# Optimization experiments

Hardware: AMD Instinct MI355X
Metric: run time of the kernel (lower is better)

Reference implementation:

```python
import jax, jax.numpy as jnp
import numpy as np
import math

D_MODEL = 512
N_HEADS = 8
D_K = D_MODEL // N_HEADS
N_SAMPLES = 16
BETA = 1.0
SCALE = 1.0 / math.sqrt(D_K)
PROPOSAL_TEMP = 0.5


def setup_inputs() -> dict:
    key = jax.random.key(0)
    ks = jax.random.split(key, 9)
    B, S = 2, 512
    x = jax.random.normal(ks[0], (B, S, D_MODEL), dtype=jnp.float32)
    init = lambda k: jax.random.normal(k, (D_MODEL, D_MODEL), dtype=jnp.float32) * 0.02
    return {
        "x": x,
        "Wq": init(ks[1]), "bq": jnp.zeros((D_MODEL,), jnp.float32),
        "Wk": init(ks[2]), "bk": jnp.zeros((D_MODEL,), jnp.float32),
        "Wv": init(ks[3]), "bv": jnp.zeros((D_MODEL,), jnp.float32),
        "Wo": init(ks[4]), "bo": jnp.zeros((D_MODEL,), jnp.float32),
    }


def _importance_sampled_weights(scores):
    # scores: [B,H,S,S]. Replicates the per-row Python loop, fully vectorized.
    B, H, Sq, Sk = scores.shape
    target = jax.nn.softmax(scores * BETA, axis=-1)            # [B,H,Sq,Sk]
    # optimal proposal: 0.5*target + 0.5*uniform
    prop = PROPOSAL_TEMP * target + (1.0 - PROPOSAL_TEMP) / Sk
    R = B * H * Sq
    tf = target.reshape(R, Sk)
    pf = prop.reshape(R, Sk)
    # tsu_backend.sample_binary_layer(log(p/(1-p))) == Bernoulli(p) sampling
    s = jax.random.bernoulli(jax.random.key(42), pf[:, None, :], (R, N_SAMPLES, Sk))
    # importance weight = prod(target[sel]) / (prod(prop[sel]) * prod(1-prop[~sel]))
    pt = jnp.prod(jnp.where(s, tf[:, None, :], 1.0), axis=-1)                 # [R,N]
    pp = jnp.prod(jnp.where(s, pf[:, None, :], 1.0 - pf[:, None, :]), axis=-1)
    valid = (s.sum(-1) > 0) & (pp > 0)
    w = jnp.where(valid, pt / jnp.maximum(pp, 1e-38), 0.0)
    ws = w.sum(-1, keepdims=True)
    w = jnp.where(ws > 0, w / jnp.maximum(ws, 1e-38), 1.0 / N_SAMPLES)        # [R,N]
    wa = jnp.einsum('rn,rnk->rk', w, s.astype(jnp.float32))                   # [R,Sk]
    was = wa.sum(-1, keepdims=True)
    wa = jnp.where(was > 0, wa / jnp.maximum(was, 1e-38), 1.0 / Sk)
    return wa.reshape(B, H, Sq, Sk)


def reference(x, Wq, bq, Wk, bk, Wv, bv, Wo, bo):
    B, S, Dm = x.shape
    proj = lambda W, b: (x @ W + b).reshape(B, S, N_HEADS, D_K).transpose(0, 2, 1, 3)
    Q = proj(Wq, bq)  # [B,H,S,dk]
    K = proj(Wk, bk)
    V = proj(Wv, bv)
    scores = jnp.einsum('bhqd,bhkd->bhqk', Q, K) * SCALE
    # torch builds weights via torch.tensor(...) which detaches => constant w.r.t. params
    attn = jax.lax.stop_gradient(_importance_sampled_weights(scores))
    out = jnp.einsum('bhqk,bhkd->bhqd', attn, V)
    out = out.transpose(0, 2, 1, 3).reshape(B, S, Dm)
    return out @ Wo + bo
```

## Files before the change

### kernel.cpp

```cpp
#include <hip/hip_runtime.h>
#include <cstdint>
#include <cstddef>


#if __has_builtin(__builtin_amdgcn_alignbit)
#define ROTL(x, r) __builtin_amdgcn_alignbit((x), (x), 32 - (r))
#else
#define ROTL(x, r) (((x) << (r)) | ((x) >> (32 - (r))))
#endif

__device__ __forceinline__ void tf4_fold(uint32_t ca, uint32_t cb, uint32_t cc,
                                         uint32_t cd, uint32_t &ra,
                                         uint32_t &rb, uint32_t &rc,
                                         uint32_t &rd) {
  uint32_t a0 = 0u, a1 = ca, b0 = 0u, b1 = cb;
  uint32_t c0 = 0u, c1 = cc, d0 = 0u, d1 = cd;
#define QR(s)                                                                 \
  a0 += a1; b0 += b1; c0 += c1; d0 += d1;                                     \
  a1 = ROTL(a1, s); b1 = ROTL(b1, s); c1 = ROTL(c1, s); d1 = ROTL(d1, s);     \
  a1 ^= a0; b1 ^= b0; c1 ^= c0; d1 ^= d0;
#define INJ(x, y)                                                             \
  a0 += (x); b0 += (x); c0 += (x); d0 += (x);                                 \
  a1 += (y); b1 += (y); c1 += (y); d1 += (y);
  QR(13) QR(15) QR(26) QR(6)
  INJ(42u, 0x1BD11BF1u)
  QR(17) QR(29) QR(16) QR(24)
  INJ(0x1BD11BF0u, 2u)
  QR(13) QR(15) QR(26) QR(6)
  a1 += 45u; b1 += 45u; c1 += 45u; d1 += 45u;
  QR(17) QR(29) QR(16) QR(24)
  INJ(42u, 0x1BD11BF4u)
  QR(13) QR(15) QR(26) QR(6)
  INJ(0x1BD11BF0u, 5u)
#undef QR
#undef INJ
  ra = a0 ^ a1; rb = b0 ^ b1; rc = c0 ^ c1; rd = d0 ^ d1;
}

__global__ __launch_bounds__(256)
void qkv_gemm(const float* __restrict__ x,
              const float* __restrict__ Wq, const float* __restrict__ bq,
              const float* __restrict__ Wk, const float* __restrict__ bk,
              const float* __restrict__ Wv, const float* __restrict__ bv,
              float* __restrict__ Qw, float* __restrict__ Kw,
              float* __restrict__ Vw) {
  const float* W; const float* bias; float* out;
  if (blockIdx.z == 0)      { W = Wq; bias = bq; out = Qw; }
  else if (blockIdx.z == 1) { W = Wk; bias = bk; out = Kw; }
  else                      { W = Wv; bias = bv; out = Vw; }

  __shared__ float At[32][68];
  __shared__ float Bs[32][64];
  const int tid = threadIdx.x;
  const int tx = tid & 15, ty = tid >> 4;
  const int row0 = blockIdx.x * 64, col0 = blockIdx.y * 64;
  float acc[4][4] = {};

  for (int kk = 0; kk < 512; kk += 32) {
    const int ar = tid >> 2;
#pragma unroll
    for (int i = 0; i < 2; ++i) {
      const int kc = ((tid & 3) << 3) + (i << 2);
      const float4 a4 =
          *(const float4*)&x[(size_t)(row0 + ar) * 512 + kk + kc];
      At[kc + 0][ar] = a4.x; At[kc + 1][ar] = a4.y;
      At[kc + 2][ar] = a4.z; At[kc + 3][ar] = a4.w;
    }
#pragma unroll
    for (int i = 0; i < 2; ++i) {
      const int idx = tid + (i << 8);
      const int br = idx >> 4, bc = (idx & 15) << 2;
      *(float4*)&Bs[br][bc] =
          *(const float4*)&W[(size_t)(kk + br) * 512 + col0 + bc];
    }
    __syncthreads();
#pragma unroll
    for (int p = 0; p < 32; ++p) {
      const float4 a4 = *(const float4*)&At[p][ty << 2];
      const float4 b4 = *(const float4*)&Bs[p][tx << 2];
      acc[0][0] = fmaf(a4.x, b4.x, acc[0][0]); acc[0][1] = fmaf(a4.x, b4.y, acc[0][1]);
      acc[0][2] = fmaf(a4.x, b4.z, acc[0][2]); acc[0][3] = fmaf(a4.x, b4.w, acc[0][3]);
      acc[1][0] = fmaf(a4.y, b4.x, acc[1][0]); acc[1][1] = fmaf(a4.y, b4.y, acc[1][1]);
      acc[1][2] = fmaf(a4.y, b4.z, acc[1][2]); acc[1][3] = fmaf(a4.y, b4.w, acc[1][3]);
      acc[2][0] = fmaf(a4.z, b4.x, acc[2][0]); acc[2][1] = fmaf(a4.z, b4.y, acc[2][1]);
      acc[2][2] = fmaf(a4.z, b4.z, acc[2][2]); acc[2][3] = fmaf(a4.z, b4.w, acc[2][3]);
      acc[3][0] = fmaf(a4.w, b4.x, acc[3][0]); acc[3][1] = fmaf(a4.w, b4.y, acc[3][1]);
      acc[3][2] = fmaf(a4.w, b4.z, acc[3][2]); acc[3][3] = fmaf(a4.w, b4.w, acc[3][3]);
    }
    __syncthreads();
  }
#pragma unroll
  for (int i = 0; i < 4; ++i) {
    const int row = row0 + (ty << 2) + i;
    const int b = row >> 9, s = row & 511;
#pragma unroll
    for (int j = 0; j < 4; ++j) {
      const int col = col0 + (tx << 2) + j;
      const int h = col >> 6, d = col & 63;
      out[(((size_t)(b * 8 + h) * 512 + s) * 64) + d] = acc[i][j] + bias[col];
    }
  }
}

__global__ __launch_bounds__(256)
void out_gemm(const float* __restrict__ A, const float* __restrict__ W,
              const float* __restrict__ bias, float* __restrict__ C) {
  __shared__ float At[32][68];
  __shared__ float Bs[32][64];
  const int tid = threadIdx.x;
  const int tx = tid & 15, ty = tid >> 4;
  const int row0 = blockIdx.x * 64, col0 = blockIdx.y * 64;
  float acc[4][4] = {};

  for (int kk = 0; kk < 512; kk += 32) {
    const int ar = tid >> 2;
#pragma unroll
    for (int i = 0; i < 2; ++i) {
      const int kc = ((tid & 3) << 3) + (i << 2);
      const float4 a4 =
          *(const float4*)&A[(size_t)(row0 + ar) * 512 + kk + kc];
      At[kc + 0][ar] = a4.x; At[kc + 1][ar] = a4.y;
      At[kc + 2][ar] = a4.z; At[kc + 3][ar] = a4.w;
    }
#pragma unroll
    for (int i = 0; i < 2; ++i) {
      const int idx = tid + (i << 8);
      const int br = idx >> 4, bc = (idx & 15) << 2;
      *(float4*)&Bs[br][bc] =
          *(const float4*)&W[(size_t)(kk + br) * 512 + col0 + bc];
    }
    __syncthreads();
#pragma unroll
    for (int p = 0; p < 32; ++p) {
      const float4 a4 = *(const float4*)&At[p][ty << 2];
      const float4 b4 = *(const float4*)&Bs[p][tx << 2];
      acc[0][0] = fmaf(a4.x, b4.x, acc[0][0]); acc[0][1] = fmaf(a4.x, b4.y, acc[0][1]);
      acc[0][2] = fmaf(a4.x, b4.z, acc[0][2]); acc[0][3] = fmaf(a4.x, b4.w, acc[0][3]);
      acc[1][0] = fmaf(a4.y, b4.x, acc[1][0]); acc[1][1] = fmaf(a4.y, b4.y, acc[1][1]);
      acc[1][2] = fmaf(a4.y, b4.z, acc[1][2]); acc[1][3] = fmaf(a4.y, b4.w, acc[1][3]);
      acc[2][0] = fmaf(a4.z, b4.x, acc[2][0]); acc[2][1] = fmaf(a4.z, b4.y, acc[2][1]);
      acc[2][2] = fmaf(a4.z, b4.z, acc[2][2]); acc[2][3] = fmaf(a4.z, b4.w, acc[2][3]);
      acc[3][0] = fmaf(a4.w, b4.x, acc[3][0]); acc[3][1] = fmaf(a4.w, b4.y, acc[3][1]);
      acc[3][2] = fmaf(a4.w, b4.z, acc[3][2]); acc[3][3] = fmaf(a4.w, b4.w, acc[3][3]);
    }
    __syncthreads();
  }
#pragma unroll
  for (int i = 0; i < 4; ++i) {
    const int row = row0 + (ty << 2) + i;
#pragma unroll
    for (int j = 0; j < 4; ++j) {
      const int col = col0 + (tx << 2) + j;
      C[(size_t)row * 512 + col] = acc[i][j] + bias[col];
    }
  }
}

__global__ __launch_bounds__(256)
void scores_softmax(const float* __restrict__ Q, const float* __restrict__ Kt,
                    float* __restrict__ tf_g) {
  const int blk = blockIdx.x;
  const int bh = blk >> 7, q0 = (blk & 127) << 2;
  const int tid = threadIdx.x;
  __shared__ __align__(16) float qs[4][64];
  __shared__ float redm[4][4], reds[4][4];
  qs[tid >> 6][tid & 63] =
      Q[((size_t)bh * 512 + q0 + (tid >> 6)) * 64 + (tid & 63)];
  __syncthreads();

  float sc[4][2];
#pragma unroll
  for (int ii = 0; ii < 2; ++ii) {
    const int k = tid + ii * 256;
    const float4* Kp = (const float4*)(Kt + ((size_t)bh * 512 + k) * 64);
    float a0 = 0.f, a1 = 0.f, a2 = 0.f, a3 = 0.f;
#pragma unroll
    for (int d4 = 0; d4 < 16; ++d4) {
      const float4 kv = Kp[d4];
      const float4 v0 = ((const float4*)qs[0])[d4];
      const float4 v1 = ((const float4*)qs[1])[d4];
      const float4 v2 = ((const float4*)qs[2])[d4];
      const float4 v3 = ((const float4*)qs[3])[d4];
      a0 = fmaf(v0.x, kv.x, a0); a0 = fmaf(v0.y, kv.y, a0);
      a0 = fmaf(v0.z, kv.z, a0); a0 = fmaf(v0.w, kv.w, a0);
      a1 = fmaf(v1.x, kv.x, a1); a1 = fmaf(v1.y, kv.y, a1);
      a1 = fmaf(v1.z, kv.z, a1); a1 = fmaf(v1.w, kv.w, a1);
      a2 = fmaf(v2.x, kv.x, a2); a2 = fmaf(v2.y, kv.y, a2);
      a2 = fmaf(v2.z, kv.z, a2); a2 = fmaf(v2.w, kv.w, a2);
      a3 = fmaf(v3.x, kv.x, a3); a3 = fmaf(v3.y, kv.y, a3);
      a3 = fmaf(v3.z, kv.z, a3); a3 = fmaf(v3.w, kv.w, a3);
    }
    sc[0][ii] = a0 * 0.125f; sc[1][ii] = a1 * 0.125f;
    sc[2][ii] = a2 * 0.125f; sc[3][ii] = a3 * 0.125f;
  }
  float mx[4];
#pragma unroll
  for (int i = 0; i < 4; ++i) mx[i] = fmaxf(sc[i][0], sc[i][1]);
  for (int m = 1; m < 64; m <<= 1) {
#pragma unroll
    for (int i = 0; i < 4; ++i) mx[i] = fmaxf(mx[i], __shfl_xor(mx[i], m));
  }
  if ((tid & 63) == 0) {
    const int w = tid >> 6;
#pragma unroll
    for (int i = 0; i < 4; ++i) redm[i][w] = mx[i];
  }
  __syncthreads();
  float ex[4][2], sm[4];
#pragma unroll
  for (int i = 0; i < 4; ++i) {
    const float rm = fmaxf(fmaxf(redm[i][0], redm[i][1]),
                           fmaxf(redm[i][2], redm[i][3]));
    ex[i][0] = expf(sc[i][0] - rm);
    ex[i][1] = expf(sc[i][1] - rm);
    sm[i] = ex[i][0] + ex[i][1];
  }
  for (int m = 1; m < 64; m <<= 1) {
#pragma unroll
    for (int i = 0; i < 4; ++i) sm[i] += __shfl_xor(sm[i], m);
  }
  if ((tid & 63) == 0) {
    const int w = tid >> 6;
#pragma unroll
    for (int i = 0; i < 4; ++i) reds[i][w] = sm[i];
  }
  __syncthreads();
#pragma unroll
  for (int i = 0; i < 4; ++i) {
    const float tot = reds[i][0] + reds[i][1] + reds[i][2] + reds[i][3];
    tf_g[((size_t)bh * 512 + q0 + i) * 512 + tid]       = ex[i][0] / tot;
    tf_g[((size_t)bh * 512 + q0 + i) * 512 + tid + 256] = ex[i][1] / tot;
  }
}

__global__ __launch_bounds__(256)
void sample_attnv(const float* __restrict__ tf_g, const float* __restrict__ V,
                  float* __restrict__ ao) {
  const int r = blockIdx.x;
  const int b = r >> 12, h = (r >> 9) & 7, q = r & 511;
  const int tid = threadIdx.x;
  __shared__ float tf[512];
  __shared__ uint32_t pscu[512];
  __shared__ float wa[512];
  __shared__ float wr[16];
  __shared__ float redc[8];
  __shared__ float psum[4][64];
  __shared__ int   list[512];
  __shared__ int   cnt;

  if (tid == 0) cnt = 0;
  {
    const float t0 = tf_g[(size_t)r * 512 + tid];
    const float t1 = tf_g[(size_t)r * 512 + tid + 256];
    tf[tid] = t0; tf[tid + 256] = t1;
    wa[tid] = 0.f; wa[tid + 256] = 0.f;
    const float p0 = fmaf(0.5f, t0, 0.0009765625f);
    const float p1 = fmaf(0.5f, t1, 0.0009765625f);
    pscu[tid]       = ((uint32_t)ceilf(p0 * 8388608.0f)) << 9;
    pscu[tid + 256] = ((uint32_t)ceilf(p1 * 8388608.0f)) << 9;
    float ql = (1.f - p0) * (1.f - p1);
    for (int m = 1; m < 64; m <<= 1) ql *= __shfl_xor(ql, m);
    if ((tid & 63) == 0) redc[4 + (tid >> 6)] = ql;
  }
  __syncthreads();
  const float Qrow = redc[4] * redc[5] * redc[6] * redc[7];

  const int n = tid >> 4, t = tid & 15;
  uint32_t pv[32];
#pragma unroll
  for (int j = 0; j < 32; ++j) pv[j] = pscu[t + (j << 4)];

  const uint32_t cnt42 =
      (uint32_t)r * 8192u + (uint32_t)n * 512u + (uint32_t)t + 42u;
  uint32_t bits = 0u;
#pragma unroll
  for (int j = 0; j < 32; j += 4) {
    uint32_t ra, rb, rc, rd;
    tf4_fold(cnt42 + (uint32_t)(j << 4), cnt42 + (uint32_t)((j + 1) << 4),
             cnt42 + (uint32_t)((j + 2) << 4), cnt42 + (uint32_t)((j + 3) << 4),
             ra, rb, rc, rd);
    bits |= (ra < pv[j] ? 1u : 0u) << j;
    bits |= (rb < pv[j + 1] ? 1u : 0u) << (j + 1);
    bits |= (rc < pv[j + 2] ? 1u : 0u) << (j + 2);
    bits |= (rd < pv[j + 3] ? 1u : 0u) << (j + 3);
  }

  float ptl = 1.f, ratl = 1.f;
  int cl = __popc(bits);
  {
    uint32_t bb = bits;
    while (bb) {
      const int j = __builtin_ctz(bb);
      bb &= bb - 1u;
      const float tv = tf[t + (j << 4)];
      const float p = fmaf(0.5f, tv, 0.0009765625f);
      ptl *= tv;
      ratl *= p / (1.f - p);
    }
  }
#pragma unroll
  for (int m = 1; m < 16; m <<= 1) {
    ptl *= __shfl_xor(ptl, m);
    ratl *= __shfl_xor(ratl, m);
    cl += __shfl_xor(cl, m);
  }
  if (t == 0) {
    const float pp = Qrow * ratl;
    wr[n] = (cl > 0 && pp > 0.f) ? (ptl / fmaxf(pp, 1e-38f)) : 0.f;
  }
  __syncthreads();
  float wsum = 0.f;
#pragma unroll
  for (int m2 = 0; m2 < 16; ++m2) wsum += wr[m2];
  const float wn = (wsum > 0.f) ? (wr[n] / fmaxf(wsum, 1e-38f)) : 0.0625f;
  {
    uint32_t bb = bits;
    while (bb) {
      const int j = __builtin_ctz(bb);
      bb &= bb - 1u;
      atomicAdd(&wa[t + (j << 4)], wn);
    }
  }
  __syncthreads();

  float sp = wa[tid] + wa[tid + 256];
  for (int m = 1; m < 64; m <<= 1) sp += __shfl_xor(sp, m);
  if ((tid & 63) == 0) redc[tid >> 6] = sp;
  if (wa[tid] > 0.f)       { const int i = atomicAdd(&cnt, 1); list[i] = tid; }
  if (wa[tid + 256] > 0.f) { const int i = atomicAdd(&cnt, 1); list[i] = tid + 256; }
  __syncthreads();
  const float was = redc[0] + redc[1] + redc[2] + redc[3];
  const int nnz = cnt;

  const int g = tid >> 6, d = tid & 63;
  const float* Vb = V + ((size_t)(b * 8 + h) * 512) * 64;
  float acc = 0.f;
  if (was > 0.f) {
    const float inv = 1.f / fmaxf(was, 1e-38f);
    for (int i = g; i < nnz; i += 4) {
      const int k = list[i];
      acc = fmaf(wa[k] * inv, Vb[(size_t)k * 64 + d], acc);
    }
  } else {
    for (int k = g; k < 512; k += 4) acc += Vb[(size_t)k * 64 + d];
    acc *= 0.001953125f;
  }
  psum[g][d] = acc;
  __syncthreads();
  if (g == 0) {
    ao[((size_t)(b * 512 + q) * 512) + h * 64 + d] =
        psum[0][d] + psum[1][d] + psum[2][d] + psum[3][d];
  }
}

extern "C" void kernel_launch(void* const* d_in, const int* in_sizes, int n_in,
                              void* d_out, int out_size, void* d_ws,
                              size_t ws_size, hipStream_t stream) {
  const float* x  = (const float*)d_in[0];
  const float* Wq = (const float*)d_in[1];
  const float* bq = (const float*)d_in[2];
  const float* Wk = (const float*)d_in[3];
  const float* bk = (const float*)d_in[4];
  const float* Wv = (const float*)d_in[5];
  const float* bv = (const float*)d_in[6];
  const float* Wo = (const float*)d_in[7];
  const float* bo = (const float*)d_in[8];
  float* out = (float*)d_out;

  float* ws = (float*)d_ws;
  float* Qw = ws;
  float* Kw = ws + 524288;
  float* Vw = ws + 1048576;
  float* tf = ws + 1572864;
  float* ao = ws + 5767168;

  dim3 gq(16, 8, 3);
  qkv_gemm<<<gq, 256, 0, stream>>>(x, Wq, bq, Wk, bk, Wv, bv, Qw, Kw, Vw);
  scores_softmax<<<2048, 256, 0, stream>>>(Qw, Kw, tf);
  sample_attnv<<<8192, 256, 0, stream>>>(tf, Vw, ao);
  dim3 go(16, 8);
  out_gemm<<<go, 256, 0, stream>>>(ao, Wo, bo, out);
}
```

Measured before the change: 307.9 us.

## Store K transposed for coalesced score loads and remap sampling to contiguous keys

The QKV GEMM now writes K in a [bh][d][s] transposed layout, so scores_softmax threads read K with coalesced per-dimension loads instead of each thread streaming its own 256-byte row. The sampling kernel also gives each thread 32 contiguous keys instead of keys strided by 16, so proposal thresholds load as uint4 vectors from LDS and tf/wa accesses become contiguous. The RNG counter is remapped to match the new key assignment, keeping the same Bernoulli stream. The transposed K store in the GEMM epilogue is strided and uncoalesced, and contiguous per-thread LDS indexing may cause bank conflicts.

```diff
diff --git a/kernel.cpp b/kernel.cpp
--- a/kernel.cpp
+++ b/kernel.cpp
@@ -42,11 +42,11 @@
               const float* __restrict__ Wq, const float* __restrict__ bq,
               const float* __restrict__ Wk, const float* __restrict__ bk,
               const float* __restrict__ Wv, const float* __restrict__ bv,
-              float* __restrict__ Qw, float* __restrict__ Kw,
+              float* __restrict__ Qw, float* __restrict__ KTw,
               float* __restrict__ Vw) {
   const float* W; const float* bias; float* out;
   if (blockIdx.z == 0)      { W = Wq; bias = bq; out = Qw; }
-  else if (blockIdx.z == 1) { W = Wk; bias = bk; out = Kw; }
+  else if (blockIdx.z == 1) { W = Wk; bias = bk; out = KTw; }
   else                      { W = Wv; bias = bv; out = Vw; }
 
   __shared__ float At[32][68];
@@ -89,6 +89,7 @@
     }
     __syncthreads();
   }
+  const bool isK = (blockIdx.z == 1);
 #pragma unroll
   for (int i = 0; i < 4; ++i) {
     const int row = row0 + (ty << 2) + i;
@@ -97,7 +98,11 @@
     for (int j = 0; j < 4; ++j) {
       const int col = col0 + (tx << 2) + j;
       const int h = col >> 6, d = col & 63;
-      out[(((size_t)(b * 8 + h) * 512 + s) * 64) + d] = acc[i][j] + bias[col];
+      const float v = acc[i][j] + bias[col];
+      if (isK)
+        out[(((size_t)(b * 8 + h) * 64 + d) * 512) + s] = v;
+      else
+        out[(((size_t)(b * 8 + h) * 512 + s) * 64) + d] = v;
     }
   }
 }
@@ -157,7 +162,7 @@
 }
 
 __global__ __launch_bounds__(256)
-void scores_softmax(const float* __restrict__ Q, const float* __restrict__ Kt,
+void scores_softmax(const float* __restrict__ Q, const float* __restrict__ KT,
                     float* __restrict__ tf_g) {
   const int blk = blockIdx.x;
   const int bh = blk >> 7, q0 = (blk & 127) << 2;
@@ -172,23 +177,26 @@
 #pragma unroll
   for (int ii = 0; ii < 2; ++ii) {
     const int k = tid + ii * 256;
-    const float4* Kp = (const float4*)(Kt + ((size_t)bh * 512 + k) * 64);
+    const float* Kp = KT + (size_t)bh * 64 * 512 + k;
     float a0 = 0.f, a1 = 0.f, a2 = 0.f, a3 = 0.f;
 #pragma unroll
     for (int d4 = 0; d4 < 16; ++d4) {
-      const float4 kv = Kp[d4];
       const float4 v0 = ((const float4*)qs[0])[d4];
       const float4 v1 = ((const float4*)qs[1])[d4];
       const float4 v2 = ((const float4*)qs[2])[d4];
       const float4 v3 = ((const float4*)qs[3])[d4];
-      a0 = fmaf(v0.x, kv.x, a0); a0 = fmaf(v0.y, kv.y, a0);
-      a0 = fmaf(v0.z, kv.z, a0); a0 = fmaf(v0.w, kv.w, a0);
-      a1 = fmaf(v1.x, kv.x, a1); a1 = fmaf(v1.y, kv.y, a1);
-      a1 = fmaf(v1.z, kv.z, a1); a1 = fmaf(v1.w, kv.w, a1);
-      a2 = fmaf(v2.x, kv.x, a2); a2 = fmaf(v2.y, kv.y, a2);
-      a2 = fmaf(v2.z, kv.z, a2); a2 = fmaf(v2.w, kv.w, a2);
-      a3 = fmaf(v3.x, kv.x, a3); a3 = fmaf(v3.y, kv.y, a3);
-      a3 = fmaf(v3.z, kv.z, a3); a3 = fmaf(v3.w, kv.w, a3);
+      const float k0 = Kp[(size_t)(d4 * 4 + 0) * 512];
+      const float k1 = Kp[(size_t)(d4 * 4 + 1) * 512];
+      const float k2 = Kp[(size_t)(d4 * 4 + 2) * 512];
+      const float k3 = Kp[(size_t)(d4 * 4 + 3) * 512];
+      a0 = fmaf(v0.x, k0, a0); a0 = fmaf(v0.y, k1, a0);
+      a0 = fmaf(v0.z, k2, a0); a0 = fmaf(v0.w, k3, a0);
+      a1 = fmaf(v1.x, k0, a1); a1 = fmaf(v1.y, k1, a1);
+      a1 = fmaf(v1.z, k2, a1); a1 = fmaf(v1.w, k3, a1);
+      a2 = fmaf(v2.x, k0, a2); a2 = fmaf(v2.y, k1, a2);
+      a2 = fmaf(v2.z, k2, a2); a2 = fmaf(v2.w, k3, a2);
+      a3 = fmaf(v3.x, k0, a3); a3 = fmaf(v3.y, k1, a3);
+      a3 = fmaf(v3.z, k2, a3); a3 = fmaf(v3.w, k3, a3);
     }
     sc[0][ii] = a0 * 0.125f; sc[1][ii] = a1 * 0.125f;
     sc[2][ii] = a2 * 0.125f; sc[3][ii] = a3 * 0.125f;
@@ -240,7 +248,7 @@
   const int b = r >> 12, h = (r >> 9) & 7, q = r & 511;
   const int tid = threadIdx.x;
   __shared__ float tf[512];
-  __shared__ uint32_t pscu[512];
+  __shared__ __align__(16) uint32_t pscu[512];
   __shared__ float wa[512];
   __shared__ float wr[16];
   __shared__ float redc[8];
@@ -266,23 +274,25 @@
   const float Qrow = redc[4] * redc[5] * redc[6] * redc[7];
 
   const int n = tid >> 4, t = tid & 15;
-  uint32_t pv[32];
-#pragma unroll
-  for (int j = 0; j < 32; ++j) pv[j] = pscu[t + (j << 4)];
-
-  const uint32_t cnt42 =
-      (uint32_t)r * 8192u + (uint32_t)n * 512u + (uint32_t)t + 42u;
+  const int k0 = t << 5;
+  uint4 pvv[8];
+#pragma unroll
+  for (int j = 0; j < 8; ++j) pvv[j] = *(const uint4*)&pscu[k0 + (j << 2)];
+
+  const uint32_t cbase =
+      (uint32_t)r * 8192u + (uint32_t)n * 512u + (uint32_t)k0 + 42u;
   uint32_t bits = 0u;
 #pragma unroll
   for (int j = 0; j < 32; j += 4) {
     uint32_t ra, rb, rc, rd;
-    tf4_fold(cnt42 + (uint32_t)(j << 4), cnt42 + (uint32_t)((j + 1) << 4),
-             cnt42 + (uint32_t)((j + 2) << 4), cnt42 + (uint32_t)((j + 3) << 4),
+    tf4_fold(cbase + (uint32_t)j, cbase + (uint32_t)j + 1u,
+             cbase + (uint32_t)j + 2u, cbase + (uint32_t)j + 3u,
              ra, rb, rc, rd);
-    bits |= (ra < pv[j] ? 1u : 0u) << j;
-    bits |= (rb < pv[j + 1] ? 1u : 0u) << (j + 1);
-    bits |= (rc < pv[j + 2] ? 1u : 0u) << (j + 2);
-    bits |= (rd < pv[j + 3] ? 1u : 0u) << (j + 3);
+    const uint4 p4 = pvv[j >> 2];
+    bits |= (ra < p4.x ? 1u : 0u) << j;
+    bits |= (rb < p4.y ? 1u : 0u) << (j + 1);
+    bits |= (rc < p4.z ? 1u : 0u) << (j + 2);
+    bits |= (rd < p4.w ? 1u : 0u) << (j + 3);
   }
 
   float ptl = 1.f, ratl = 1.f;
@@ -292,7 +302,7 @@
     while (bb) {
       const int j = __builtin_ctz(bb);
       bb &= bb - 1u;
-      const float tv = tf[t + (j << 4)];
+      const float tv = tf[k0 + j];
       const float p = fmaf(0.5f, tv, 0.0009765625f);
       ptl *= tv;
       ratl *= p / (1.f - p);
@@ -318,7 +328,7 @@
     while (bb) {
       const int j = __builtin_ctz(bb);
       bb &= bb - 1u;
-      atomicAdd(&wa[t + (j << 4)], wn);
+      atomicAdd(&wa[k0 + j], wn);
     }
   }
   __syncthreads();
@@ -369,14 +379,14 @@
 
   float* ws = (float*)d_ws;
   float* Qw = ws;
-  float* Kw = ws + 524288;
+  float* KT = ws + 524288;
   float* Vw = ws + 1048576;
   float* tf = ws + 1572864;
   float* ao = ws + 5767168;
 
   dim3 gq(16, 8, 3);
-  qkv_gemm<<<gq, 256, 0, stream>>>(x, Wq, bq, Wk, bk, Wv, bv, Qw, Kw, Vw);
-  scores_softmax<<<2048, 256, 0, stream>>>(Qw, Kw, tf);
+  qkv_gemm<<<gq, 256, 0, stream>>>(x, Wq, bq, Wk, bk, Wv, bv, Qw, KT, Vw);
+  scores_softmax<<<2048, 256, 0, stream>>>(Qw, KT, tf);
   sample_attnv<<<8192, 256, 0, stream>>>(tf, Vw, ao);
   dim3 go(16, 8);
   out_gemm<<<go, 256, 0, stream>>>(ao, Wo, bo, out);
```

Result: faster. 273.1 us (-11.3%).
